# Kernel optimization log

Measured on AMD Instinct MI355X. Metric: run time of the kernel, lower is better.

Reference implementation:

```python
import jax, jax.numpy as jnp
import numpy as np

IN_DIM, COND_DIM, OUT_DIM = 256, 256, 128
B, LQ, LK = 4, 4096, 4096


def setup_inputs() -> dict:
    key = jax.random.key(0)
    ks = jax.random.split(key, 8)
    s_in = 1.0 / np.sqrt(IN_DIM)
    s_c = 1.0 / np.sqrt(COND_DIM)
    return {
        "x": jax.random.normal(ks[0], (B, LQ, IN_DIM), dtype=jnp.float32),
        "cond": jax.random.normal(ks[1], (B, LK, COND_DIM), dtype=jnp.float32),
        "Wq": jax.random.uniform(ks[2], (IN_DIM, OUT_DIM), jnp.float32, -s_in, s_in),
        "bq": jax.random.uniform(ks[3], (OUT_DIM,), jnp.float32, -s_in, s_in),
        "Wk": jax.random.uniform(ks[4], (COND_DIM, OUT_DIM), jnp.float32, -s_c, s_c),
        "bk": jax.random.uniform(ks[5], (OUT_DIM,), jnp.float32, -s_c, s_c),
        "Wv": jax.random.uniform(ks[6], (COND_DIM, OUT_DIM), jnp.float32, -s_c, s_c),
        "bv": jax.random.uniform(ks[7], (OUT_DIM,), jnp.float32, -s_c, s_c),
    }


def reference(x, cond, Wq, bq, Wk, bk, Wv, bv):
    # q: [B, Lq, D], k/v: [B, Lk, D]
    q = jnp.einsum("bqi,id->bqd", x, Wq) + bq
    k = jnp.einsum("bkc,cd->bkd", cond, Wk) + bk
    v = jnp.einsum("bkc,cd->bkd", cond, Wv) + bv
    # NOTE: original uses UNscaled dot product (no 1/sqrt(d)).
    scores = jnp.einsum("bqd,bkd->bqk", q, k)  # [B, Lq, Lk]
    attn = jax.nn.softmax(scores, axis=-1)
    return jnp.einsum("bqk,bkd->bqd", attn, v)  # [B, Lq, D]
```

## Files before the change

### kernel.cpp

```cpp
#include <hip/hip_runtime.h>
#include <hip/hip_bf16.h>


typedef __attribute__((ext_vector_type(8))) short short8;
typedef __attribute__((ext_vector_type(8))) unsigned short ushort8;
typedef __attribute__((ext_vector_type(4))) unsigned short us4;
typedef __attribute__((ext_vector_type(4))) float f32x4;
typedef __attribute__((ext_vector_type(16))) float f32x16;
typedef __attribute__((ext_vector_type(4))) unsigned int u32x4;
typedef __bf16 bf16x8 __attribute__((ext_vector_type(8)));

constexpr int BATCH  = 4;
constexpr int SEQLEN = 4096;
constexpr int DIN    = 256;
constexpr int DOUT   = 128;
constexpr int ROWS   = BATCH * SEQLEN;

static __device__ __forceinline__ unsigned short bf16_rn(float f) {
  unsigned int u = __builtin_bit_cast(unsigned int, f);
  unsigned int r = u + 0x7FFFu + ((u >> 16) & 1u);
  return (unsigned short)(r >> 16);
}
static __device__ __forceinline__ float bf16_f32(unsigned short h) {
  return __builtin_bit_cast(float, (unsigned int)h << 16);
}

static __device__ __forceinline__ f32x4 mfma_bf16(short8 a, short8 b, f32x4 c) {
  return __builtin_amdgcn_mfma_f32_16x16x32_bf16(
      __builtin_bit_cast(bf16x8, a), __builtin_bit_cast(bf16x8, b), c, 0, 0, 0);
}
static __device__ __forceinline__ f32x16 mfma32(short8 a, short8 b, f32x16 c) {
  return __builtin_amdgcn_mfma_f32_32x32x16_bf16(
      __builtin_bit_cast(bf16x8, a), __builtin_bit_cast(bf16x8, b), c, 0, 0, 0);
}

static __device__ __forceinline__ unsigned int cvt_pk(float lo, float hi) {
  unsigned int r;
  asm("v_cvt_pk_bf16_f32 %0, %1, %2" : "=v"(r) : "v"(lo), "v"(hi));
  return r;
}
static __device__ __forceinline__ void permswap(unsigned int& a, unsigned int& b) {
  asm("v_permlane32_swap_b32 %0, %1" : "+v"(a), "+v"(b));
}

static __device__ __forceinline__ int swz128(int a) {
  return a ^ (((a >> 7) & 7) << 4);
}


__global__ __launch_bounds__(256) void proj_kernel(
    const float* __restrict__ x, const float* __restrict__ cond,
    const float* __restrict__ Wq, const float* __restrict__ bq,
    const float* __restrict__ Wk, const float* __restrict__ bk,
    const float* __restrict__ Wv, const float* __restrict__ bv,
    unsigned short* __restrict__ qb, unsigned short* __restrict__ kb,
    unsigned short* __restrict__ vt)
{
  const int which = blockIdx.y;
  const float* __restrict__ src  = (which == 0) ? x  : cond;
  const float* __restrict__ W    = (which == 0) ? Wq : (which == 1 ? Wk : Wv);
  const float* __restrict__ bias = (which == 0) ? bq : (which == 1 ? bk : bv);
  const int r0 = blockIdx.x * 64;

  __shared__ __align__(16) char lds[32768];
  char* const AhB = lds;
  char* const AlB = lds + 8192;
  char* const WtB = lds + 16384;

  const int tid  = threadIdx.x;
  const int wv   = tid >> 6;
  const int lane = tid & 63;
  const int g    = lane >> 4;
  const int c    = lane & 15;

  f32x4 acc[8];
  #pragma unroll
  for (int cf = 0; cf < 8; ++cf) acc[cf] = (f32x4){0.f, 0.f, 0.f, 0.f};

  for (int kt = 0; kt < 4; ++kt) {
    #pragma unroll
    for (int i = 0; i < 4; ++i) {
      const int idx = tid + i * 256;
      const int row = idx >> 4, f4 = idx & 15;
      const float4 a4 =
          *(const float4*)(src + (size_t)(r0 + row) * DIN + kt * 64 + f4 * 4);
      us4 hi, lo;
      const float av[4] = {a4.x, a4.y, a4.z, a4.w};
      #pragma unroll
      for (int e = 0; e < 4; ++e) {
        hi[e] = bf16_rn(av[e]);
        lo[e] = bf16_rn(av[e] - bf16_f32(hi[e]));
      }
      const int off = swz128(row * 128 + f4 * 8);
      *(us4*)(AhB + off) = hi;
      *(us4*)(AlB + off) = lo;
    }
    {
      const int col = tid & 127, half = tid >> 7;
      #pragma unroll
      for (int j = 0; j < 4; ++j) {
        const int k0 = half * 32 + j * 8;
        ushort8 wb;
        #pragma unroll
        for (int e = 0; e < 8; ++e)
          wb[e] = bf16_rn(W[(size_t)(kt * 64 + k0 + e) * DOUT + col]);
        *(ushort8*)(WtB + swz128(col * 128 + k0 * 2)) = wb;
      }
    }
    __syncthreads();

    #pragma unroll
    for (int ks = 0; ks < 2; ++ks) {
      const int aoff = (wv * 16 + c) * 128 + ks * 64 + g * 16;
      const short8 ah = *(const short8*)(AhB + swz128(aoff));
      const short8 al = *(const short8*)(AlB + swz128(aoff));
      #pragma unroll
      for (int cf = 0; cf < 8; ++cf) {
        const short8 wb =
            *(const short8*)(WtB + swz128((cf * 16 + c) * 128 + ks * 64 + g * 16));
        acc[cf] = mfma_bf16(ah, wb, acc[cf]);
        acc[cf] = mfma_bf16(al, wb, acc[cf]);
      }
    }
    __syncthreads();
  }

  if (which == 0) {
    #pragma unroll
    for (int cf = 0; cf < 8; ++cf) {
      const float bb = bias[cf * 16 + c];
      #pragma unroll
      for (int r = 0; r < 4; ++r)
        qb[(size_t)(r0 + wv * 16 + g * 4 + r) * DOUT + cf * 16 + c] =
            bf16_rn(acc[cf][r] + bb);
    }
  } else if (which == 1) {
    const int rowbase = r0 + wv * 16 + g * 4;
    const int h = (c >> 3) & 1, e = c & 7;
    #pragma unroll
    for (int cf = 0; cf < 8; ++cf) {
      const float bb = bias[cf * 16 + c];
      #pragma unroll
      for (int r = 0; r < 4; ++r) {
        const int row  = rowbase + r;
        const int b2   = row >> 12;
        const int kblk = (row & 4095) >> 5;
        const int l31  = row & 31;
        kb[((((size_t)b2 * 128 + kblk) * 8 + cf) * 64 + h * 32 + l31) * 8 + e] =
            bf16_rn(acc[cf][r] + bb);
      }
    }
  } else {
    const int keybase = r0 + wv * 16 + g * 4;
    const int b2   = keybase >> 12;
    const int kblk = (keybase & 4095) >> 5;
    const int kk   = (keybase >> 4) & 1;
    const int h    = (keybase >> 3) & 1;
    const int e0   = keybase & 7;
    #pragma unroll
    for (int cf = 0; cf < 8; ++cf) {
      const float bb = bias[cf * 16 + c];
      const int col  = cf * 16 + c;
      const int dblk = col >> 5, l31 = col & 31;
      us4 pk;
      #pragma unroll
      for (int r = 0; r < 4; ++r) pk[r] = bf16_rn(acc[cf][r] + bb);
      *(us4*)(vt + (((((size_t)b2 * 128 + kblk) * 4 + dblk) * 2 + kk) * 64 +
                    h * 32 + l31) * 8 + e0) = pk;
    }
  }
}

constexpr int NSPLIT = 4;
constexpr int QBLK   = 32;
constexpr int KVBLK  = 32;
constexpr int ITERS  = SEQLEN / NSPLIT / KVBLK;

__global__ __launch_bounds__(256, 2) void attn_kernel(
    const unsigned short* __restrict__ qb,
    const unsigned short* __restrict__ kb,
    const unsigned short* __restrict__ vt,
    float* __restrict__ out)
{
  __shared__ __align__(16) float cmb[2][32][132];
  __shared__ float Ml[NSPLIT][32][2];

  const int bid = ((blockIdx.x & 7) << 6) | (blockIdx.x >> 3);
  const int qt  = bid & 127;
  const int b   = bid >> 7;
  const int tid = threadIdx.x;
  const int split = tid >> 6;
  const int lane  = tid & 63;
  const int ql = lane & 31;
  const int h  = lane >> 5;

  const int q0 = qt * QBLK;

  short8 qf[8];
  {
    const char* qp = (const char*)(qb + (size_t)(b * SEQLEN + q0 + ql) * DOUT) + h * 16;
    #pragma unroll
    for (int f = 0; f < 8; ++f) qf[f] = *(const short8*)(qp + f * 32);
  }

  const int kblk0 = split * (SEQLEN / NSPLIT / 32);
  const char* kfb = (const char*)kb + ((size_t)b * 128 + kblk0) * 8192 + lane * 16;
  const char* vfb = (const char*)vt + ((size_t)b * 128 + kblk0) * 8192 + lane * 16;

  f32x16 acc[4];
  #pragma unroll
  for (int d = 0; d < 4; ++d)
    #pragma unroll
    for (int r = 0; r < 16; ++r) acc[d][r] = 0.f;
  float mc = -1e30f, lc = 0.f;

  short8 kf[8], vf[4][2];
  #pragma unroll
  for (int f = 0; f < 8; ++f) kf[f] = *(const short8*)(kfb + f * 1024);
  #pragma unroll
  for (int d = 0; d < 4; ++d)
    #pragma unroll
    for (int kk = 0; kk < 2; ++kk)
      vf[d][kk] = *(const short8*)(vfb + (d * 2 + kk) * 1024);

  for (int t = 0; t < ITERS; ++t) {
    const bool more = (t + 1 < ITERS);

    f32x16 s;
    #pragma unroll
    for (int r = 0; r < 16; ++r) s[r] = 0.f;
    __builtin_amdgcn_s_setprio(1);
    #pragma unroll
    for (int f = 0; f < 8; ++f) s = mfma32(kf[f], qf[f], s);
    __builtin_amdgcn_s_setprio(0);

    if (more) {
      kfb += 8192;
      #pragma unroll
      for (int f = 0; f < 8; ++f) kf[f] = *(const short8*)(kfb + f * 1024);
    }

    float tm = s[0];
    #pragma unroll
    for (int r = 1; r < 16; ++r) tm = fmaxf(tm, s[r]);
    if (!__all(tm <= mc + 8.f)) {
      float tr = fmaxf(tm, __shfl_xor(tm, 32));
      const float mnew  = fmaxf(mc, tr);
      const float sc    = __expf(mc - mnew);
      mc = mnew;
      lc *= sc;
      #pragma unroll
      for (int d = 0; d < 4; ++d)
        #pragma unroll
        for (int r = 0; r < 16; ++r) acc[d][r] *= sc;
    }
    float p[16];
    float rs = 0.f;
    #pragma unroll
    for (int r = 0; r < 16; ++r) {
      p[r] = __expf(s[r] - mc);
      rs += p[r];
    }
    lc += rs;

    short8 pfrag[2];
    #pragma unroll
    for (int kk = 0; kk < 2; ++kk) {
      unsigned int A  = cvt_pk(p[kk * 8 + 0], p[kk * 8 + 1]);
      unsigned int Bv = cvt_pk(p[kk * 8 + 2], p[kk * 8 + 3]);
      unsigned int C  = cvt_pk(p[kk * 8 + 4], p[kk * 8 + 5]);
      unsigned int Dv = cvt_pk(p[kk * 8 + 6], p[kk * 8 + 7]);
      permswap(A, C);
      permswap(Bv, Dv);
      const u32x4 w = {A, Bv, C, Dv};
      pfrag[kk] = __builtin_bit_cast(short8, w);
    }

    __builtin_amdgcn_s_setprio(1);
    #pragma unroll
    for (int d = 0; d < 4; ++d)
      #pragma unroll
      for (int kk = 0; kk < 2; ++kk)
        acc[d] = mfma32(vf[d][kk], pfrag[kk], acc[d]);
    __builtin_amdgcn_s_setprio(0);

    if (more) {
      vfb += 8192;
      #pragma unroll
      for (int d = 0; d < 4; ++d)
        #pragma unroll
        for (int kk = 0; kk < 2; ++kk)
          vf[d][kk] = *(const short8*)(vfb + (d * 2 + kk) * 1024);
    }
  }

  lc += __shfl_xor(lc, 32);
  if (lane < 32) { Ml[split][ql][0] = mc; Ml[split][ql][1] = lc; }
  __syncthreads();

  float mg = -1e30f, lsum = 0.f;
  #pragma unroll
  for (int s2 = 0; s2 < NSPLIT; ++s2) mg = fmaxf(mg, Ml[s2][ql][0]);
  #pragma unroll
  for (int s2 = 0; s2 < NSPLIT; ++s2)
    lsum += Ml[s2][ql][1] * __expf(Ml[s2][ql][0] - mg);
  const float fac = __expf(mc - mg);
  #pragma unroll
  for (int d = 0; d < 4; ++d)
    #pragma unroll
    for (int r = 0; r < 16; ++r) acc[d][r] *= fac;

  if (split & 1) {
    float* reg = &cmb[split >> 1][0][0];
    #pragma unroll
    for (int d = 0; d < 4; ++d)
      #pragma unroll
      for (int rr = 0; rr < 4; ++rr) {
        const f32x4 v = {acc[d][rr*4+0], acc[d][rr*4+1], acc[d][rr*4+2], acc[d][rr*4+3]};
        *(f32x4*)(reg + ql * 132 + d * 32 + rr * 8 + h * 4) = v;
      }
  }
  __syncthreads();
  if (!(split & 1)) {
    const float* reg = &cmb[split >> 1][0][0];
    #pragma unroll
    for (int d = 0; d < 4; ++d)
      #pragma unroll
      for (int rr = 0; rr < 4; ++rr) {
        const f32x4 v = *(const f32x4*)(reg + ql * 132 + d * 32 + rr * 8 + h * 4);
        acc[d][rr*4+0] += v.x; acc[d][rr*4+1] += v.y;
        acc[d][rr*4+2] += v.z; acc[d][rr*4+3] += v.w;
      }
  }
  __syncthreads();
  if (split == 2) {
    float* reg = &cmb[0][0][0];
    #pragma unroll
    for (int d = 0; d < 4; ++d)
      #pragma unroll
      for (int rr = 0; rr < 4; ++rr) {
        const f32x4 v = {acc[d][rr*4+0], acc[d][rr*4+1], acc[d][rr*4+2], acc[d][rr*4+3]};
        *(f32x4*)(reg + ql * 132 + d * 32 + rr * 8 + h * 4) = v;
      }
  }
  __syncthreads();
  if (split == 0) {
    const float* reg = &cmb[0][0][0];
    const float inv = 1.f / lsum;
    float* const op = out + (size_t)(b * SEQLEN + q0 + ql) * DOUT;
    #pragma unroll
    for (int d = 0; d < 4; ++d)
      #pragma unroll
      for (int rr = 0; rr < 4; ++rr) {
        const f32x4 v = *(const f32x4*)(reg + ql * 132 + d * 32 + rr * 8 + h * 4);
        f32x4 o;
        o.x = (acc[d][rr*4+0] + v.x) * inv;
        o.y = (acc[d][rr*4+1] + v.y) * inv;
        o.z = (acc[d][rr*4+2] + v.z) * inv;
        o.w = (acc[d][rr*4+3] + v.w) * inv;
        *(f32x4*)(op + d * 32 + rr * 8 + h * 4) = o;
      }
  }
}

extern "C" void kernel_launch(void* const* d_in, const int* in_sizes, int n_in,
                              void* d_out, int out_size, void* d_ws, size_t ws_size,
                              hipStream_t stream) {
  const float* x    = (const float*)d_in[0];
  const float* cond = (const float*)d_in[1];
  const float* Wq   = (const float*)d_in[2];
  const float* bq   = (const float*)d_in[3];
  const float* Wk   = (const float*)d_in[4];
  const float* bk   = (const float*)d_in[5];
  const float* Wv   = (const float*)d_in[6];
  const float* bv   = (const float*)d_in[7];
  float* out = (float*)d_out;

  unsigned short* qb = (unsigned short*)d_ws;
  unsigned short* kb = qb + (size_t)ROWS * DOUT;
  unsigned short* vt = kb + (size_t)ROWS * DOUT;

  proj_kernel<<<dim3(ROWS / 64, 3), 256, 0, stream>>>(
      x, cond, Wq, bq, Wk, bk, Wv, bv, qb, kb, vt);

  attn_kernel<<<dim3(BATCH * (SEQLEN / QBLK)), 256, 0, stream>>>(
      qb, kb, vt, out);
}
```

Measured before the change: 75.05 us.

## Use 1024-thread attention blocks with two q-subtiles and 8-way KV split

The attention kernel now runs 1024-thread blocks covering 64 queries as two 32-query subtiles, each split 8 ways over the KV sequence, and merges partials with a tree reduction through shared memory. This halves the block count and doubles per-query KV parallelism, aiming to improve occupancy and latency hiding on the long KV loop, at the cost of a more expensive cross-wave reduction with many barriers. Separately, the K projection output is staged through a swizzled LDS tile so global writes become coalesced 16-byte stores instead of scattered 2-byte stores.

```diff
diff --git a/kernel.cpp b/kernel.cpp
--- a/kernel.cpp
+++ b/kernel.cpp
@@ -45,6 +45,9 @@
 
 static __device__ __forceinline__ int swz128(int a) {
   return a ^ (((a >> 7) & 7) << 4);
+}
+static __device__ __forceinline__ int swzK(int a) {
+  return a ^ (((a >> 8) & 15) << 4);
 }
 
 
@@ -135,20 +138,32 @@
             bf16_rn(acc[cf][r] + bb);
     }
   } else if (which == 1) {
-    const int rowbase = r0 + wv * 16 + g * 4;
-    const int h = (c >> 3) & 1, e = c & 7;
+    char* const Ktile = lds;
     #pragma unroll
     for (int cf = 0; cf < 8; ++cf) {
       const float bb = bias[cf * 16 + c];
       #pragma unroll
       for (int r = 0; r < 4; ++r) {
-        const int row  = rowbase + r;
-        const int b2   = row >> 12;
-        const int kblk = (row & 4095) >> 5;
-        const int l31  = row & 31;
-        kb[((((size_t)b2 * 128 + kblk) * 8 + cf) * 64 + h * 32 + l31) * 8 + e] =
+        const int row = wv * 16 + g * 4 + r;
+        *(unsigned short*)(Ktile + swzK(row * 256 + (cf * 16 + c) * 2)) =
             bf16_rn(acc[cf][r] + bb);
       }
+    }
+    __syncthreads();
+    const int b2     = r0 >> 12;
+    const int kblkG0 = (r0 & 4095) >> 5;
+    #pragma unroll
+    for (int j = 0; j < 4; ++j) {
+      const int i    = tid + j * 256;
+      const int kblk = i >> 9;
+      const int rem  = i & 511;
+      const int f    = rem >> 6;
+      const int ln   = rem & 63;
+      const int row  = kblk * 32 + (ln & 31);
+      const int colb = f * 32 + (ln >> 5) * 16;
+      const ushort8 v = *(const ushort8*)(Ktile + swzK(row * 256 + colb));
+      *(ushort8*)((char*)kb +
+          (((size_t)(b2 * 128 + kblkG0 + kblk) * 8 + f) * 64 + ln) * 16) = v;
     }
   } else {
     const int keybase = r0 + wv * 16 + g * 4;
@@ -171,30 +186,31 @@
   }
 }
 
-constexpr int NSPLIT = 4;
-constexpr int QBLK   = 32;
+constexpr int NSPLIT = 8;
 constexpr int KVBLK  = 32;
 constexpr int ITERS  = SEQLEN / NSPLIT / KVBLK;
 
-__global__ __launch_bounds__(256, 2) void attn_kernel(
+__global__ __launch_bounds__(1024, 4) void attn_kernel(
     const unsigned short* __restrict__ qb,
     const unsigned short* __restrict__ kb,
     const unsigned short* __restrict__ vt,
     float* __restrict__ out)
 {
-  __shared__ __align__(16) float cmb[2][32][132];
-  __shared__ float Ml[NSPLIT][32][2];
-
-  const int bid = ((blockIdx.x & 7) << 6) | (blockIdx.x >> 3);
-  const int qt  = bid & 127;
-  const int b   = bid >> 7;
+  __shared__ __align__(16) float cmbPool[4][32][132];
+  __shared__ float Ml[2][NSPLIT][32][2];
+
+  const int bid = ((blockIdx.x & 7) << 5) | (blockIdx.x >> 3);
+  const int qt  = bid & 63;
+  const int b   = bid >> 6;
   const int tid = threadIdx.x;
-  const int split = tid >> 6;
+  const int wid   = tid >> 6;
+  const int qsub  = wid & 1;
+  const int split = wid >> 1;
   const int lane  = tid & 63;
   const int ql = lane & 31;
   const int h  = lane >> 5;
 
-  const int q0 = qt * QBLK;
+  const int q0 = qt * 64 + qsub * 32;
 
   short8 qf[8];
   {
@@ -295,23 +311,22 @@
   }
 
   lc += __shfl_xor(lc, 32);
-  if (lane < 32) { Ml[split][ql][0] = mc; Ml[split][ql][1] = lc; }
+  if (lane < 32) { Ml[qsub][split][ql][0] = mc; Ml[qsub][split][ql][1] = lc; }
   __syncthreads();
 
   float mg = -1e30f, lsum = 0.f;
   #pragma unroll
-  for (int s2 = 0; s2 < NSPLIT; ++s2) mg = fmaxf(mg, Ml[s2][ql][0]);
+  for (int s2 = 0; s2 < NSPLIT; ++s2) mg = fmaxf(mg, Ml[qsub][s2][ql][0]);
   #pragma unroll
   for (int s2 = 0; s2 < NSPLIT; ++s2)
-    lsum += Ml[s2][ql][1] * __expf(Ml[s2][ql][0] - mg);
+    lsum += Ml[qsub][s2][ql][1] * __expf(Ml[qsub][s2][ql][0] - mg);
   const float fac = __expf(mc - mg);
   #pragma unroll
   for (int d = 0; d < 4; ++d)
     #pragma unroll
     for (int r = 0; r < 16; ++r) acc[d][r] *= fac;
 
-  if (split & 1) {
-    float* reg = &cmb[split >> 1][0][0];
+  auto writeReg = [&](float* reg) {
     #pragma unroll
     for (int d = 0; d < 4; ++d)
       #pragma unroll
@@ -319,10 +334,8 @@
         const f32x4 v = {acc[d][rr*4+0], acc[d][rr*4+1], acc[d][rr*4+2], acc[d][rr*4+3]};
         *(f32x4*)(reg + ql * 132 + d * 32 + rr * 8 + h * 4) = v;
       }
-  }
-  __syncthreads();
-  if (!(split & 1)) {
-    const float* reg = &cmb[split >> 1][0][0];
+  };
+  auto addReg = [&](const float* reg) {
     #pragma unroll
     for (int d = 0; d < 4; ++d)
       #pragma unroll
@@ -331,35 +344,38 @@
         acc[d][rr*4+0] += v.x; acc[d][rr*4+1] += v.y;
         acc[d][rr*4+2] += v.z; acc[d][rr*4+3] += v.w;
       }
-  }
-  __syncthreads();
-  if (split == 2) {
-    float* reg = &cmb[0][0][0];
-    #pragma unroll
-    for (int d = 0; d < 4; ++d)
-      #pragma unroll
-      for (int rr = 0; rr < 4; ++rr) {
-        const f32x4 v = {acc[d][rr*4+0], acc[d][rr*4+1], acc[d][rr*4+2], acc[d][rr*4+3]};
-        *(f32x4*)(reg + ql * 132 + d * 32 + rr * 8 + h * 4) = v;
-      }
-  }
-  __syncthreads();
-  if (split == 0) {
-    const float* reg = &cmb[0][0][0];
-    const float inv = 1.f / lsum;
-    float* const op = out + (size_t)(b * SEQLEN + q0 + ql) * DOUT;
-    #pragma unroll
-    for (int d = 0; d < 4; ++d)
-      #pragma unroll
-      for (int rr = 0; rr < 4; ++rr) {
-        const f32x4 v = *(const f32x4*)(reg + ql * 132 + d * 32 + rr * 8 + h * 4);
-        f32x4 o;
-        o.x = (acc[d][rr*4+0] + v.x) * inv;
-        o.y = (acc[d][rr*4+1] + v.y) * inv;
-        o.z = (acc[d][rr*4+2] + v.z) * inv;
-        o.w = (acc[d][rr*4+3] + v.w) * inv;
-        *(f32x4*)(op + d * 32 + rr * 8 + h * 4) = o;
-      }
+  };
+
+  #pragma unroll
+  for (int qs = 0; qs < 2; ++qs) {
+    const bool me = (qsub == qs);
+    if (me && split >= 4) writeReg(&cmbPool[split - 4][0][0]);
+    __syncthreads();
+    if (me && split < 4) addReg(&cmbPool[split][0][0]);
+    __syncthreads();
+    if (me && (split == 2 || split == 3)) writeReg(&cmbPool[split - 2][0][0]);
+    __syncthreads();
+    if (me && split < 2) addReg(&cmbPool[split][0][0]);
+    __syncthreads();
+    if (me && split == 1) writeReg(&cmbPool[0][0][0]);
+    __syncthreads();
+    if (me && split == 0) {
+      addReg(&cmbPool[0][0][0]);
+      const float inv = 1.f / lsum;
+      float* const op = out + (size_t)(b * SEQLEN + q0 + ql) * DOUT;
+      #pragma unroll
+      for (int d = 0; d < 4; ++d)
+        #pragma unroll
+        for (int rr = 0; rr < 4; ++rr) {
+          f32x4 o;
+          o.x = acc[d][rr*4+0] * inv;
+          o.y = acc[d][rr*4+1] * inv;
+          o.z = acc[d][rr*4+2] * inv;
+          o.w = acc[d][rr*4+3] * inv;
+          *(f32x4*)(op + d * 32 + rr * 8 + h * 4) = o;
+        }
+    }
+    if (qs == 0) __syncthreads();
   }
 }
 
@@ -383,6 +399,6 @@
   proj_kernel<<<dim3(ROWS / 64, 3), 256, 0, stream>>>(
       x, cond, Wq, bq, Wk, bk, Wv, bv, qb, kb, vt);
 
-  attn_kernel<<<dim3(BATCH * (SEQLEN / QBLK)), 256, 0, stream>>>(
+  attn_kernel<<<dim3(BATCH * (SEQLEN / 64)), 1024, 0, stream>>>(
       qb, kb, vt, out);
 }
```

Result: slower. 276.1 us (+267.9%).
